# Performance work log

Hardware: AMD Instinct MI355X
Metric: run time of the kernel (lower is better)

## Reference

```python
import jax, jax.numpy as jnp
import numpy as np

DIM = 1024
HEADS = 16
THS = 0.5  # deterministic threshold gating (forward called with ths=0.5)
C = float(np.e) * float(np.sqrt(1.0 / DIM))  # MaskedLinear init constant


def _pm_c(key, shape):
    # weights drawn from {-c, +c}, as in MaskedLinear 'mask' mode
    return jnp.where(jax.random.bernoulli(key, 0.5, shape), C, -C).astype(jnp.float32)


def setup_inputs() -> dict:
    key = jax.random.key(0)
    ks = jax.random.split(key, 7)
    b, n = 2, 2048
    return {
        "x": jax.random.normal(ks[0], (b, n, DIM), jnp.float32),
        "qkv_weight": _pm_c(ks[1], (3 * DIM, DIM)),
        "qkv_weight_mask": jax.random.normal(ks[2], (3 * DIM, DIM), jnp.float32),
        "out_weight": _pm_c(ks[3], (DIM, DIM)),
        "out_weight_mask": jax.random.normal(ks[4], (DIM, DIM), jnp.float32),
        "out_bias": _pm_c(ks[5], (DIM,)),
        "out_bias_mask": jax.random.normal(ks[6], (DIM,), jnp.float32),
    }


def reference(x, qkv_weight, qkv_weight_mask, out_weight, out_weight_mask,
              out_bias, out_bias_mask):
    b, n, _ = x.shape
    h, d = HEADS, DIM // HEADS
    dt = x.dtype

    # MaskedLinear (no bias): gate = 1[sigmoid(mask) > ths]
    g_qkv = (jax.nn.sigmoid(qkv_weight_mask) > THS).astype(dt)
    qkv = jnp.einsum('bnk,ok->bno', x, g_qkv * qkv_weight)  # [b, n, 3*dim]

    # rearrange 'b n (qkv h d) -> qkv b h n d'
    qkv = qkv.reshape(b, n, 3, h, d)
    q, k, v = (jnp.transpose(qkv[:, :, i], (0, 2, 1, 3)) for i in range(3))

    scale = DIM ** (-0.5)  # NOTE: full dim, matches source
    dots = jnp.einsum('bhid,bhjd->bhij', q, k) * scale  # [b, h, n, n]
    attn = jax.nn.softmax(dots, axis=-1)
    out = jnp.einsum('bhij,bhjd->bhid', attn, v)  # [b, h, n, d]
    out = jnp.transpose(out, (0, 2, 1, 3)).reshape(b, n, h * d)

    # MaskedLinear with bias
    g_w = (jax.nn.sigmoid(out_weight_mask) > THS).astype(dt)
    g_b = (jax.nn.sigmoid(out_bias_mask) > THS).astype(dt)
    out = jnp.einsum('bnk,ok->bno', out, g_w * out_weight) + g_b * out_bias
    # dropout: eval mode -> identity
    return out
```

## Files before the change

### kernel.cpp

```cpp
#include <hip/hip_runtime.h>

#define HEADS 16
#define DH 64
#define SEQ 2048
#define MROWS 4096
#define KDIM 1024
#define N3 3072

#define C_D (2.718281828459045 * 0.03125)
#define C_F ((float)C_D)
#define QSCALE ((float)(C_D * C_D / 32.0))

typedef __attribute__((ext_vector_type(8))) short bf16x8;
typedef __attribute__((ext_vector_type(4))) short s16x4;
typedef __attribute__((ext_vector_type(4))) float f32x4;
#define MFMA16 __builtin_amdgcn_mfma_f32_16x16x32_bf16

__device__ __forceinline__ unsigned short f2bf(float f) {
  unsigned int u = __float_as_uint(f);
  unsigned int r = u + 0x7FFFu + ((u >> 16) & 1u);
  return (unsigned short)(r >> 16);
}
__device__ __forceinline__ float bf2f(unsigned short h) {
  return __uint_as_float(((unsigned int)h) << 16);
}
__device__ __forceinline__ unsigned int split2u(float v) {
  const unsigned short hh = f2bf(v);
  const unsigned short ll = f2bf(v - bf2f(hh));
  return (unsigned int)hh | ((unsigned int)ll << 16);
}

__global__ __launch_bounds__(256) void sign_gate(const float* __restrict__ w,
                                                 const float* __restrict__ m,
                                                 unsigned short* __restrict__ s,
                                                 int n4) {
  const int i = blockIdx.x * 256 + threadIdx.x;
  if (i >= n4) return;
  const float4 wv = ((const float4*)w)[i];
  const float4 mv = ((const float4*)m)[i];
  s16x4 r;
  r[0] = (mv.x > 0.f) ? (wv.x > 0.f ? (short)0x3F80 : (short)0xBF80) : (short)0;
  r[1] = (mv.y > 0.f) ? (wv.y > 0.f ? (short)0x3F80 : (short)0xBF80) : (short)0;
  r[2] = (mv.z > 0.f) ? (wv.z > 0.f ? (short)0x3F80 : (short)0xBF80) : (short)0;
  r[3] = (mv.w > 0.f) ? (wv.w > 0.f ? (short)0x3F80 : (short)0xBF80) : (short)0;
  ((s16x4*)s)[i] = r;
}

template <int MODE>
__global__ __launch_bounds__(256) void gemm_mfma(
    const float* __restrict__ A, const unsigned short* __restrict__ Bsgn,
    const float* __restrict__ bias, const float* __restrict__ bias_m,
    float* __restrict__ qo, float* __restrict__ ko, float* __restrict__ vto,
    float* __restrict__ oo, int M, int N, int K) {
  __shared__ unsigned short Ah[128 * 40];
  __shared__ unsigned short Al[128 * 40];
  __shared__ unsigned short Bt[128 * 40];
  const int tid = threadIdx.x;
  const int l = tid & 63;
  const int w = tid >> 6;
  const int lr = l & 15, lg = l >> 4;
  const int wr = w >> 1, wc = w & 1;
  const int bm = blockIdx.y * 128, bn = blockIdx.x * 128;

  f32x4 acc[4][4];
#pragma unroll
  for (int i = 0; i < 4; ++i)
#pragma unroll
    for (int j = 0; j < 4; ++j)
#pragma unroll
      for (int r = 0; r < 4; ++r) acc[i][j][r] = 0.f;

  for (int k0 = 0; k0 < K; k0 += 32) {
    __syncthreads();
#pragma unroll
    for (int p = 0; p < 4; ++p) {
      const int ch = tid + p * 256;
      const int r = ch >> 3, c = ch & 7;
      const float4 f = *(const float4*)&A[(size_t)(bm + r) * K + k0 + c * 4];
      const unsigned int p0 = split2u(f.x), p1 = split2u(f.y),
                         p2 = split2u(f.z), p3 = split2u(f.w);
      s16x4 hv, lv;
      hv[0] = (short)(p0 & 0xFFFFu); lv[0] = (short)(p0 >> 16);
      hv[1] = (short)(p1 & 0xFFFFu); lv[1] = (short)(p1 >> 16);
      hv[2] = (short)(p2 & 0xFFFFu); lv[2] = (short)(p2 >> 16);
      hv[3] = (short)(p3 & 0xFFFFu); lv[3] = (short)(p3 >> 16);
      *(s16x4*)&Ah[r * 40 + c * 4] = hv;
      *(s16x4*)&Al[r * 40 + c * 4] = lv;
    }
#pragma unroll
    for (int p = 0; p < 2; ++p) {
      const int ch = tid + p * 256;
      const int r = ch >> 2, c = ch & 3;
      const uint4 u = *(const uint4*)&Bsgn[(size_t)(bn + r) * K + k0 + c * 8];
      *(uint4*)&Bt[r * 40 + c * 8] = u;
    }
    __syncthreads();

    bf16x8 af[4], alf[4], bfr[4];
#pragma unroll
    for (int i = 0; i < 4; ++i) {
      const int row = wr * 64 + i * 16 + lr;
      af[i] = *(const bf16x8*)&Ah[row * 40 + lg * 8];
      alf[i] = *(const bf16x8*)&Al[row * 40 + lg * 8];
    }
#pragma unroll
    for (int j = 0; j < 4; ++j)
      bfr[j] = *(const bf16x8*)&Bt[(wc * 64 + j * 16 + lr) * 40 + lg * 8];
#pragma unroll
    for (int i = 0; i < 4; ++i)
#pragma unroll
      for (int j = 0; j < 4; ++j) {
        acc[i][j] = MFMA16(af[i], bfr[j], acc[i][j], 0, 0, 0);
        acc[i][j] = MFMA16(alf[i], bfr[j], acc[i][j], 0, 0, 0);
      }
  }

  if (MODE == 0) {
    const int part = bn >> 10;
    const int rembase = bn & 1023;
#pragma unroll
    for (int i = 0; i < 4; ++i)
#pragma unroll
      for (int j = 0; j < 4; ++j) {
        const int gcol = rembase + wc * 64 + j * 16 + lr;
        const int h = gcol >> 6, d = gcol & 63;
#pragma unroll
        for (int r = 0; r < 4; ++r) {
          const int grow = bm + wr * 64 + i * 16 + lg * 4 + r;
          const int b = grow >> 11, n = grow & 2047;
          const int bh = b * HEADS + h;
          const float v = acc[i][j][r];
          if (part == 0)
            qo[((size_t)bh * SEQ + n) * DH + d] = v * QSCALE;
          else if (part == 1)
            ko[((size_t)bh * SEQ + n) * DH + d] = v;
          else
            vto[((size_t)bh * DH + d) * SEQ + n] = v * C_F;
        }
      }
  } else {
#pragma unroll
    for (int j = 0; j < 4; ++j) {
      const int gcol = bn + wc * 64 + j * 16 + lr;
      const float bg = (bias_m[gcol] > 0.f) ? bias[gcol] : 0.f;
#pragma unroll
      for (int i = 0; i < 4; ++i)
#pragma unroll
        for (int r = 0; r < 4; ++r) {
          const int grow = bm + wr * 64 + i * 16 + lg * 4 + r;
          oo[(size_t)grow * N + gcol] = acc[i][j][r] * C_F + bg;
        }
    }
  }
}

__global__ __launch_bounds__(256) void attn_mfma(const float* __restrict__ q,
                                                 const float* __restrict__ kk,
                                                 const float* __restrict__ vt,
                                                 float* __restrict__ ao) {
  __shared__ unsigned short Kh[64 * 72];
  __shared__ unsigned short Kl[64 * 72];
  __shared__ unsigned short Vh[64 * 72];
  __shared__ unsigned short Vl[64 * 72];
  __shared__ unsigned short Ph[4][16 * 72];
  __shared__ unsigned short Pl[4][16 * 72];

  const int tid = threadIdx.x;
  const int l = tid & 63;
  const int w = tid >> 6;
  const int lr = l & 15, lg = l >> 4;
  const int qt = blockIdx.x;
  const int bh = blockIdx.y;

  const float* qb = q + (size_t)bh * SEQ * DH;
  const float* kb = kk + (size_t)bh * SEQ * DH;
  const float* vb = vt + (size_t)bh * DH * SEQ;

  bf16x8 qh[2], ql[2];
  const int q0 = qt * 64 + w * 16;
#pragma unroll
  for (int s = 0; s < 2; ++s) {
    const float* src = &qb[(size_t)(q0 + lr) * DH + s * 32 + lg * 8];
    const float4 f0 = *(const float4*)src;
    const float4 f1 = *(const float4*)(src + 4);
    const float fv[8] = {f0.x, f0.y, f0.z, f0.w, f1.x, f1.y, f1.z, f1.w};
    bf16x8 h, lo;
#pragma unroll
    for (int jj = 0; jj < 8; ++jj) {
      const unsigned int pp = split2u(fv[jj]);
      h[jj] = (short)(pp & 0xFFFFu);
      lo[jj] = (short)(pp >> 16);
    }
    qh[s] = h;
    ql[s] = lo;
  }

  f32x4 oacc[4];
  float m_i[4], l_i[4];
#pragma unroll
  for (int dt = 0; dt < 4; ++dt)
#pragma unroll
    for (int r = 0; r < 4; ++r) oacc[dt][r] = 0.f;
#pragma unroll
  for (int r = 0; r < 4; ++r) {
    m_i[r] = -1e30f;
    l_i[r] = 0.f;
  }

  for (int kt = 0; kt < SEQ / 64; ++kt) {
    __syncthreads();
#pragma unroll
    for (int p = 0; p < 4; ++p) {
      const int ch = tid + p * 256;
      const int r = ch >> 4, c = ch & 15;
      const float4 f = *(const float4*)&kb[(size_t)(kt * 64 + r) * DH + c * 4];
      {
        const unsigned int p0 = split2u(f.x), p1 = split2u(f.y),
                           p2 = split2u(f.z), p3 = split2u(f.w);
        s16x4 hv, lv;
        hv[0] = (short)(p0 & 0xFFFFu); lv[0] = (short)(p0 >> 16);
        hv[1] = (short)(p1 & 0xFFFFu); lv[1] = (short)(p1 >> 16);
        hv[2] = (short)(p2 & 0xFFFFu); lv[2] = (short)(p2 >> 16);
        hv[3] = (short)(p3 & 0xFFFFu); lv[3] = (short)(p3 >> 16);
        *(s16x4*)&Kh[r * 72 + c * 4] = hv;
        *(s16x4*)&Kl[r * 72 + c * 4] = lv;
      }
      const float4 g = *(const float4*)&vb[(size_t)r * SEQ + kt * 64 + c * 4];
      {
        const unsigned int p0 = split2u(g.x), p1 = split2u(g.y),
                           p2 = split2u(g.z), p3 = split2u(g.w);
        s16x4 hv, lv;
        hv[0] = (short)(p0 & 0xFFFFu); lv[0] = (short)(p0 >> 16);
        hv[1] = (short)(p1 & 0xFFFFu); lv[1] = (short)(p1 >> 16);
        hv[2] = (short)(p2 & 0xFFFFu); lv[2] = (short)(p2 >> 16);
        hv[3] = (short)(p3 & 0xFFFFu); lv[3] = (short)(p3 >> 16);
        *(s16x4*)&Vh[r * 72 + c * 4] = hv;
        *(s16x4*)&Vl[r * 72 + c * 4] = lv;
      }
    }
    __syncthreads();

    f32x4 sacc[4];
#pragma unroll
    for (int ct = 0; ct < 4; ++ct)
#pragma unroll
      for (int r = 0; r < 4; ++r) sacc[ct][r] = 0.f;
#pragma unroll
    for (int ct = 0; ct < 4; ++ct)
#pragma unroll
      for (int s = 0; s < 2; ++s) {
        const int off = (ct * 16 + lr) * 72 + s * 32 + lg * 8;
        const bf16x8 kh = *(const bf16x8*)&Kh[off];
        const bf16x8 kl = *(const bf16x8*)&Kl[off];
        sacc[ct] = MFMA16(qh[s], kh, sacc[ct], 0, 0, 0);
        sacc[ct] = MFMA16(qh[s], kl, sacc[ct], 0, 0, 0);
        sacc[ct] = MFMA16(ql[s], kh, sacc[ct], 0, 0, 0);
      }

    float ps[4][4], alpha[4];
#pragma unroll
    for (int r = 0; r < 4; ++r) {
      float mx = fmaxf(fmaxf(sacc[0][r], sacc[1][r]),
                       fmaxf(sacc[2][r], sacc[3][r]));
#pragma unroll
      for (int off = 1; off < 16; off <<= 1) mx = fmaxf(mx, __shfl_xor(mx, off));
      const float mn = fmaxf(m_i[r], mx);
      alpha[r] = __expf(m_i[r] - mn);
      float rs = 0.f;
#pragma unroll
      for (int ct = 0; ct < 4; ++ct) {
        ps[ct][r] = __expf(sacc[ct][r] - mn);
        rs += ps[ct][r];
      }
#pragma unroll
      for (int off = 1; off < 16; off <<= 1) rs += __shfl_xor(rs, off);
      l_i[r] = l_i[r] * alpha[r] + rs;
      m_i[r] = mn;
    }

#pragma unroll
    for (int ct = 0; ct < 4; ++ct)
#pragma unroll
      for (int r = 0; r < 4; ++r) {
        const unsigned short h = f2bf(ps[ct][r]);
        Ph[w][(lg * 4 + r) * 72 + ct * 16 + lr] = h;
        Pl[w][(lg * 4 + r) * 72 + ct * 16 + lr] =
            f2bf(ps[ct][r] - bf2f(h));
      }

#pragma unroll
    for (int dt = 0; dt < 4; ++dt)
#pragma unroll
      for (int r = 0; r < 4; ++r) oacc[dt][r] *= alpha[r];

#pragma unroll
    for (int s = 0; s < 2; ++s) {
      const bf16x8 ph = *(const bf16x8*)&Ph[w][lr * 72 + s * 32 + lg * 8];
      const bf16x8 pl = *(const bf16x8*)&Pl[w][lr * 72 + s * 32 + lg * 8];
#pragma unroll
      for (int dt = 0; dt < 4; ++dt) {
        const int off = (dt * 16 + lr) * 72 + s * 32 + lg * 8;
        const bf16x8 vh = *(const bf16x8*)&Vh[off];
        const bf16x8 vl = *(const bf16x8*)&Vl[off];
        oacc[dt] = MFMA16(ph, vh, oacc[dt], 0, 0, 0);
        oacc[dt] = MFMA16(ph, vl, oacc[dt], 0, 0, 0);
        oacc[dt] = MFMA16(pl, vh, oacc[dt], 0, 0, 0);
      }
    }
  }

  const int b = bh >> 4, hh = bh & 15;
#pragma unroll
  for (int r = 0; r < 4; ++r) {
    const float inv = 1.f / l_i[r];
    const int n = qt * 64 + w * 16 + lg * 4 + r;
#pragma unroll
    for (int dt = 0; dt < 4; ++dt)
      ao[((size_t)(b * SEQ + n)) * KDIM + hh * DH + dt * 16 + lr] =
          oacc[dt][r] * inv;
  }
}

extern "C" void kernel_launch(void* const* d_in, const int* in_sizes, int n_in,
                              void* d_out, int out_size, void* d_ws,
                              size_t ws_size, hipStream_t stream) {
  const float* x = (const float*)d_in[0];
  const float* qkvw = (const float*)d_in[1];
  const float* qkvm = (const float*)d_in[2];
  const float* outw = (const float*)d_in[3];
  const float* outm = (const float*)d_in[4];
  const float* ob = (const float*)d_in[5];
  const float* obm = (const float*)d_in[6];
  float* out = (float*)d_out;

  float* q = (float*)d_ws;
  float* kv = q + (size_t)MROWS * KDIM;
  float* vt = kv + (size_t)MROWS * KDIM;
  float* ao = vt + (size_t)MROWS * KDIM;
  unsigned short* sq = (unsigned short*)ao;
  unsigned short* so = (unsigned short*)q;

  sign_gate<<<dim3(N3 * KDIM / 4 / 256), 256, 0, stream>>>(qkvw, qkvm, sq,
                                                           N3 * KDIM / 4);
  gemm_mfma<0><<<dim3(N3 / 128, MROWS / 128), 256, 0, stream>>>(
      x, sq, nullptr, nullptr, q, kv, vt, nullptr, MROWS, N3, KDIM);
  attn_mfma<<<dim3(SEQ / 64, 32), 256, 0, stream>>>(q, kv, vt, ao);
  sign_gate<<<dim3(KDIM * KDIM / 4 / 256), 256, 0, stream>>>(outw, outm, so,
                                                             KDIM * KDIM / 4);
  gemm_mfma<1><<<dim3(KDIM / 128, MROWS / 128), 256, 0, stream>>>(
      ao, so, ob, obm, nullptr, nullptr, nullptr, out, MROWS, KDIM, KDIM);
}
```

Baseline: 495.8 us.

## Pre-split activations into bf16 hi/lo pairs in producer epilogues

The QKV GEMM epilogue now emits Q as packed hi/lo bf16 words and K and V^T as separate hi and lo bf16 planes. The attention epilogue likewise writes packed hi/lo output for the final GEMM. This removes the repeated fp32-to-bf16 splitting inside the attention K/V tile loads, which every query block redid for every key tile, and inside the output GEMM A loads. Global traffic per element stays about the same (two bf16 instead of one fp32), while the attention inner loop loses ALU work. The cost is more, scattered 16-bit stores in the QKV epilogue and a new fixed-offset workspace layout.

Measured after the change: 426.0 us. 1.16x faster.

```diff
diff --git a/kernel.cpp b/kernel.cpp
--- a/kernel.cpp
+++ b/kernel.cpp
@@ -48,9 +48,11 @@
 
 template <int MODE>
 __global__ __launch_bounds__(256) void gemm_mfma(
-    const float* __restrict__ A, const unsigned short* __restrict__ Bsgn,
-    const float* __restrict__ bias, const float* __restrict__ bias_m,
-    float* __restrict__ qo, float* __restrict__ ko, float* __restrict__ vto,
+    const float* __restrict__ Af, const unsigned int* __restrict__ Apk,
+    const unsigned short* __restrict__ Bsgn, const float* __restrict__ bias,
+    const float* __restrict__ bias_m, unsigned int* __restrict__ qpk,
+    unsigned short* __restrict__ khg, unsigned short* __restrict__ klg,
+    unsigned short* __restrict__ vthg, unsigned short* __restrict__ vtlg,
     float* __restrict__ oo, int M, int N, int K) {
   __shared__ unsigned short Ah[128 * 40];
   __shared__ unsigned short Al[128 * 40];
@@ -76,14 +78,22 @@
     for (int p = 0; p < 4; ++p) {
       const int ch = tid + p * 256;
       const int r = ch >> 3, c = ch & 7;
-      const float4 f = *(const float4*)&A[(size_t)(bm + r) * K + k0 + c * 4];
-      const unsigned int p0 = split2u(f.x), p1 = split2u(f.y),
-                         p2 = split2u(f.z), p3 = split2u(f.w);
       s16x4 hv, lv;
-      hv[0] = (short)(p0 & 0xFFFFu); lv[0] = (short)(p0 >> 16);
-      hv[1] = (short)(p1 & 0xFFFFu); lv[1] = (short)(p1 >> 16);
-      hv[2] = (short)(p2 & 0xFFFFu); lv[2] = (short)(p2 >> 16);
-      hv[3] = (short)(p3 & 0xFFFFu); lv[3] = (short)(p3 >> 16);
+      if (MODE == 0) {
+        const float4 f = *(const float4*)&Af[(size_t)(bm + r) * K + k0 + c * 4];
+        const unsigned int p0 = split2u(f.x), p1 = split2u(f.y),
+                           p2 = split2u(f.z), p3 = split2u(f.w);
+        hv[0] = (short)(p0 & 0xFFFFu); lv[0] = (short)(p0 >> 16);
+        hv[1] = (short)(p1 & 0xFFFFu); lv[1] = (short)(p1 >> 16);
+        hv[2] = (short)(p2 & 0xFFFFu); lv[2] = (short)(p2 >> 16);
+        hv[3] = (short)(p3 & 0xFFFFu); lv[3] = (short)(p3 >> 16);
+      } else {
+        const uint4 u = *(const uint4*)&Apk[(size_t)(bm + r) * K + k0 + c * 4];
+        hv[0] = (short)(u.x & 0xFFFFu); lv[0] = (short)(u.x >> 16);
+        hv[1] = (short)(u.y & 0xFFFFu); lv[1] = (short)(u.y >> 16);
+        hv[2] = (short)(u.z & 0xFFFFu); lv[2] = (short)(u.z >> 16);
+        hv[3] = (short)(u.w & 0xFFFFu); lv[3] = (short)(u.w >> 16);
+      }
       *(s16x4*)&Ah[r * 40 + c * 4] = hv;
       *(s16x4*)&Al[r * 40 + c * 4] = lv;
     }
@@ -130,12 +140,19 @@
           const int b = grow >> 11, n = grow & 2047;
           const int bh = b * HEADS + h;
           const float v = acc[i][j][r];
-          if (part == 0)
-            qo[((size_t)bh * SEQ + n) * DH + d] = v * QSCALE;
-          else if (part == 1)
-            ko[((size_t)bh * SEQ + n) * DH + d] = v;
-          else
-            vto[((size_t)bh * DH + d) * SEQ + n] = v * C_F;
+          if (part == 0) {
+            qpk[((size_t)bh * SEQ + n) * DH + d] = split2u(v * QSCALE);
+          } else if (part == 1) {
+            const unsigned int u = split2u(v);
+            const size_t idx = ((size_t)bh * SEQ + n) * DH + d;
+            khg[idx] = (unsigned short)(u & 0xFFFFu);
+            klg[idx] = (unsigned short)(u >> 16);
+          } else {
+            const unsigned int u = split2u(v * C_F);
+            const size_t idx = ((size_t)bh * DH + d) * SEQ + n;
+            vthg[idx] = (unsigned short)(u & 0xFFFFu);
+            vtlg[idx] = (unsigned short)(u >> 16);
+          }
         }
       }
   } else {
@@ -154,10 +171,11 @@
   }
 }
 
-__global__ __launch_bounds__(256) void attn_mfma(const float* __restrict__ q,
-                                                 const float* __restrict__ kk,
-                                                 const float* __restrict__ vt,
-                                                 float* __restrict__ ao) {
+__global__ __launch_bounds__(256) void attn_mfma(
+    const unsigned int* __restrict__ qpk, const unsigned short* __restrict__ khg,
+    const unsigned short* __restrict__ klg,
+    const unsigned short* __restrict__ vthg,
+    const unsigned short* __restrict__ vtlg, unsigned int* __restrict__ aopk) {
   __shared__ unsigned short Kh[64 * 72];
   __shared__ unsigned short Kl[64 * 72];
   __shared__ unsigned short Vh[64 * 72];
@@ -172,25 +190,22 @@
   const int qt = blockIdx.x;
   const int bh = blockIdx.y;
 
-  const float* qb = q + (size_t)bh * SEQ * DH;
-  const float* kb = kk + (size_t)bh * SEQ * DH;
-  const float* vb = vt + (size_t)bh * DH * SEQ;
-
   bf16x8 qh[2], ql[2];
   const int q0 = qt * 64 + w * 16;
+  const unsigned int* qrow = &qpk[((size_t)bh * SEQ + q0 + lr) * DH];
 #pragma unroll
   for (int s = 0; s < 2; ++s) {
-    const float* src = &qb[(size_t)(q0 + lr) * DH + s * 32 + lg * 8];
-    const float4 f0 = *(const float4*)src;
-    const float4 f1 = *(const float4*)(src + 4);
-    const float fv[8] = {f0.x, f0.y, f0.z, f0.w, f1.x, f1.y, f1.z, f1.w};
+    const uint4 u0 = *(const uint4*)&qrow[s * 32 + lg * 8];
+    const uint4 u1 = *(const uint4*)&qrow[s * 32 + lg * 8 + 4];
     bf16x8 h, lo;
-#pragma unroll
-    for (int jj = 0; jj < 8; ++jj) {
-      const unsigned int pp = split2u(fv[jj]);
-      h[jj] = (short)(pp & 0xFFFFu);
-      lo[jj] = (short)(pp >> 16);
-    }
+    h[0] = (short)(u0.x & 0xFFFFu); lo[0] = (short)(u0.x >> 16);
+    h[1] = (short)(u0.y & 0xFFFFu); lo[1] = (short)(u0.y >> 16);
+    h[2] = (short)(u0.z & 0xFFFFu); lo[2] = (short)(u0.z >> 16);
+    h[3] = (short)(u0.w & 0xFFFFu); lo[3] = (short)(u0.w >> 16);
+    h[4] = (short)(u1.x & 0xFFFFu); lo[4] = (short)(u1.x >> 16);
+    h[5] = (short)(u1.y & 0xFFFFu); lo[5] = (short)(u1.y >> 16);
+    h[6] = (short)(u1.z & 0xFFFFu); lo[6] = (short)(u1.z >> 16);
+    h[7] = (short)(u1.w & 0xFFFFu); lo[7] = (short)(u1.w >> 16);
     qh[s] = h;
     ql[s] = lo;
   }
@@ -210,33 +225,15 @@
   for (int kt = 0; kt < SEQ / 64; ++kt) {
     __syncthreads();
 #pragma unroll
-    for (int p = 0; p < 4; ++p) {
+    for (int p = 0; p < 2; ++p) {
       const int ch = tid + p * 256;
-      const int r = ch >> 4, c = ch & 15;
-      const float4 f = *(const float4*)&kb[(size_t)(kt * 64 + r) * DH + c * 4];
-      {
-        const unsigned int p0 = split2u(f.x), p1 = split2u(f.y),
-                           p2 = split2u(f.z), p3 = split2u(f.w);
-        s16x4 hv, lv;
-        hv[0] = (short)(p0 & 0xFFFFu); lv[0] = (short)(p0 >> 16);
-        hv[1] = (short)(p1 & 0xFFFFu); lv[1] = (short)(p1 >> 16);
-        hv[2] = (short)(p2 & 0xFFFFu); lv[2] = (short)(p2 >> 16);
-        hv[3] = (short)(p3 & 0xFFFFu); lv[3] = (short)(p3 >> 16);
-        *(s16x4*)&Kh[r * 72 + c * 4] = hv;
-        *(s16x4*)&Kl[r * 72 + c * 4] = lv;
-      }
-      const float4 g = *(const float4*)&vb[(size_t)r * SEQ + kt * 64 + c * 4];
-      {
-        const unsigned int p0 = split2u(g.x), p1 = split2u(g.y),
-                           p2 = split2u(g.z), p3 = split2u(g.w);
-        s16x4 hv, lv;
-        hv[0] = (short)(p0 & 0xFFFFu); lv[0] = (short)(p0 >> 16);
-        hv[1] = (short)(p1 & 0xFFFFu); lv[1] = (short)(p1 >> 16);
-        hv[2] = (short)(p2 & 0xFFFFu); lv[2] = (short)(p2 >> 16);
-        hv[3] = (short)(p3 & 0xFFFFu); lv[3] = (short)(p3 >> 16);
-        *(s16x4*)&Vh[r * 72 + c * 4] = hv;
-        *(s16x4*)&Vl[r * 72 + c * 4] = lv;
-      }
+      const int r = ch >> 3, c = ch & 7;
+      const size_t kidx = ((size_t)bh * SEQ + kt * 64 + r) * DH + c * 8;
+      const size_t vidx = ((size_t)bh * DH + r) * SEQ + kt * 64 + c * 8;
+      *(uint4*)&Kh[r * 72 + c * 8] = *(const uint4*)&khg[kidx];
+      *(uint4*)&Kl[r * 72 + c * 8] = *(const uint4*)&klg[kidx];
+      *(uint4*)&Vh[r * 72 + c * 8] = *(const uint4*)&vthg[vidx];
+      *(uint4*)&Vl[r * 72 + c * 8] = *(const uint4*)&vtlg[vidx];
     }
     __syncthreads();
 
@@ -284,8 +281,7 @@
       for (int r = 0; r < 4; ++r) {
         const unsigned short h = f2bf(ps[ct][r]);
         Ph[w][(lg * 4 + r) * 72 + ct * 16 + lr] = h;
-        Pl[w][(lg * 4 + r) * 72 + ct * 16 + lr] =
-            f2bf(ps[ct][r] - bf2f(h));
+        Pl[w][(lg * 4 + r) * 72 + ct * 16 + lr] = f2bf(ps[ct][r] - bf2f(h));
       }
 
 #pragma unroll
@@ -316,8 +312,8 @@
     const int n = qt * 64 + w * 16 + lg * 4 + r;
 #pragma unroll
     for (int dt = 0; dt < 4; ++dt)
-      ao[((size_t)(b * SEQ + n)) * KDIM + hh * DH + dt * 16 + lr] =
-          oacc[dt][r] * inv;
+      aopk[((size_t)(b * SEQ + n)) * KDIM + hh * DH + dt * 16 + lr] =
+          split2u(oacc[dt][r] * inv);
   }
 }
 
@@ -333,20 +329,26 @@
   const float* obm = (const float*)d_in[6];
   float* out = (float*)d_out;
 
-  float* q = (float*)d_ws;
-  float* kv = q + (size_t)MROWS * KDIM;
-  float* vt = kv + (size_t)MROWS * KDIM;
-  float* ao = vt + (size_t)MROWS * KDIM;
-  unsigned short* sq = (unsigned short*)ao;
-  unsigned short* so = (unsigned short*)q;
+  char* base = (char*)d_ws;
+  unsigned int* qpk = (unsigned int*)base;
+  unsigned short* khg = (unsigned short*)(base + (16u << 20));
+  unsigned short* klg = (unsigned short*)(base + (24u << 20));
+  unsigned short* vthg = (unsigned short*)(base + (32u << 20));
+  unsigned short* vtlg = (unsigned short*)(base + (40u << 20));
+  unsigned int* aopk = (unsigned int*)(base + (48u << 20));
+  unsigned short* sq = (unsigned short*)aopk;
+  unsigned short* so = (unsigned short*)qpk;
 
   sign_gate<<<dim3(N3 * KDIM / 4 / 256), 256, 0, stream>>>(qkvw, qkvm, sq,
                                                            N3 * KDIM / 4);
   gemm_mfma<0><<<dim3(N3 / 128, MROWS / 128), 256, 0, stream>>>(
-      x, sq, nullptr, nullptr, q, kv, vt, nullptr, MROWS, N3, KDIM);
-  attn_mfma<<<dim3(SEQ / 64, 32), 256, 0, stream>>>(q, kv, vt, ao);
+      x, nullptr, sq, nullptr, nullptr, qpk, khg, klg, vthg, vtlg, nullptr,
+      MROWS, N3, KDIM);
+  attn_mfma<<<dim3(SEQ / 64, 32), 256, 0, stream>>>(qpk, khg, klg, vthg, vtlg,
+                                                    aopk);
   sign_gate<<<dim3(KDIM * KDIM / 4 / 256), 256, 0, stream>>>(outw, outm, so,
                                                              KDIM * KDIM / 4);
   gemm_mfma<1><<<dim3(KDIM / 128, MROWS / 128), 256, 0, stream>>>(
-      ao, so, ob, obm, nullptr, nullptr, nullptr, out, MROWS, KDIM, KDIM);
-}
+      nullptr, aopk, so, ob, obm, nullptr, nullptr, nullptr, nullptr, nullptr,
+      out, MROWS, KDIM, KDIM);
+}
```
